# Kernel optimization log

Hardware: AMD Instinct MI355X
Metric: run time of the kernel (lower is better)

The kernel has to match this reference:

```python
import jax, jax.numpy as jnp
import numpy as np

B, S, HID = 2, 2048, 4096
H, KVH, D = 32, 8, 128
MAXPOS = 4096


def _rotate_half(x):
    x1, x2 = jnp.split(x, 2, axis=-1)
    return jnp.concatenate([-x2, x1], axis=-1)


def setup_inputs() -> dict:
    key = jax.random.key(0)
    k0, k1, k2, k3, k4 = jax.random.split(key, 5)
    s = 0.02
    hidden_states = jax.random.normal(k0, (B, S, HID), jnp.float32)
    Wq = jax.random.normal(k1, (HID, H * D), jnp.float32) * s
    Wk = jax.random.normal(k2, (HID, KVH * D), jnp.float32) * s
    Wv = jax.random.normal(k3, (HID, KVH * D), jnp.float32) * s
    Wo = jax.random.normal(k4, (H * D, HID), jnp.float32) * s
    past_key_value = jnp.zeros((B, 2, KVH, MAXPOS, D), jnp.float32)
    # RoPE tables (fp32, as asserted in the torch module)
    inv_freq = 1.0 / (10000.0 ** (np.arange(0, D, 2, dtype=np.float64) / D))
    freqs = np.outer(np.arange(S, dtype=np.float64), inv_freq)  # [S, D/2]
    emb = np.concatenate([freqs, freqs], axis=-1)                # [S, D]
    cos = jnp.asarray(np.cos(emb), jnp.float32)
    sin = jnp.asarray(np.sin(emb), jnp.float32)
    return {"hidden_states": hidden_states, "past_key_value": past_key_value,
            "cos": cos, "sin": sin, "Wq": Wq, "Wk": Wk, "Wv": Wv, "Wo": Wo}


def reference(hidden_states, past_key_value, cos, sin, Wq, Wk, Wv, Wo):
    b, s, _ = hidden_states.shape
    # QKV projections (no bias, as in Llama-style attention)
    q = (hidden_states @ Wq).reshape(b, s, H, D)
    k = (hidden_states @ Wk).reshape(b, s, KVH, D)
    v = (hidden_states @ Wv).reshape(b, s, KVH, D)
    # Fused RoPE (qk_norm is identity for standard models)
    c = cos[None, :, None, :]
    sn = sin[None, :, None, :]
    q = q * c + _rotate_half(q) * sn
    k = k * c + _rotate_half(k) * sn
    # KV-cache update (prefill: context_lengths=0, kvcache_start_index=0)
    k_bhsd = k.transpose(0, 2, 1, 3)  # [b, kvh, s, d]
    v_bhsd = v.transpose(0, 2, 1, 3)
    present = past_key_value.at[:, 0, :, :s, :].set(k_bhsd)
    present = present.at[:, 1, :, :s, :].set(v_bhsd)
    # GQA: repeat kv heads to match query heads
    rep = H // KVH
    kr = jnp.repeat(k, rep, axis=2)  # [b, s, H, d]
    vr = jnp.repeat(v, rep, axis=2)
    scores = jnp.einsum("bqhd,bkhd->bhqk", q, kr) / np.float32(np.sqrt(D))
    causal = jnp.tril(jnp.ones((s, s), bool))  # [q, k]
    scores = jnp.where(causal[None, None], scores, jnp.finfo(scores.dtype).min)
    w = jax.nn.softmax(scores.astype(jnp.float32), axis=-1).astype(q.dtype)
    attn = jnp.einsum("bhqk,bkhd->bqhd", w, vr).reshape(b, s, H * D)
    out = attn @ Wo
    return out, present
```

## Files before the change

kernel.cpp:

```cpp
#include <hip/hip_runtime.h>
#include <hip/hip_bf16.h>

typedef unsigned short u16;
typedef __bf16 bf16x8 __attribute__((ext_vector_type(8)));
typedef float  f32x4  __attribute__((ext_vector_type(4)));

__device__ __forceinline__ u16 f2bf(float f) {
    return __builtin_bit_cast(u16, (__bf16)f);
}
__device__ __forceinline__ float b2f(u16 u) {
    return __builtin_bit_cast(float, (unsigned)u << 16);
}
__device__ __forceinline__ f32x4 mfma16(bf16x8 a, bf16x8 b, f32x4 c) {
    return __builtin_amdgcn_mfma_f32_16x16x32_bf16(a, b, c, 0, 0, 0);
}
__device__ __forceinline__ void gl_lds16(const void* g, void* l) {
    __builtin_amdgcn_global_load_lds((const __attribute__((address_space(1))) void*)g,
                                     (__attribute__((address_space(3))) void*)l, 16, 0, 0);
}

__global__ void k_pre(const float* __restrict__ hidden, u16* __restrict__ hiddenB,
                      const float4* __restrict__ past, float4* __restrict__ present4) {
    int bx = blockIdx.x;
    if (bx < 16384) {
        long i = ((long)bx * 256 + threadIdx.x) * 4;
        float4 v = *(const float4*)(hidden + i);
        ushort4 o;
        o.x = f2bf(v.x); o.y = f2bf(v.y); o.z = f2bf(v.z); o.w = f2bf(v.w);
        *(ushort4*)(hiddenB + i) = o;
    } else {
        long i = (long)(bx - 16384) * 256 + threadIdx.x;
        long g = i >> 16;
        long inner = i & 65535;
        long off = g * 131072 + 65536 + inner;
        present4[off] = past[off];
    }
}

__global__ void k_transpose_all(const float* __restrict__ Wq, const float* __restrict__ Wk,
                                const float* __restrict__ Wv, const float* __restrict__ Wo,
                                u16* __restrict__ WqkvT, u16* __restrict__ WoT) {
    __shared__ float t[32][33];
    const int bx = blockIdx.x, k0 = blockIdx.y * 32;
    const float* src; u16* dst; int N; int col;
    if (bx < 128)      { src = Wq; N = 4096; col = bx * 32;         dst = WqkvT; }
    else if (bx < 160) { src = Wk; N = 1024; col = (bx - 128) * 32; dst = WqkvT + 4096L * 4096; }
    else if (bx < 192) { src = Wv; N = 1024; col = (bx - 160) * 32; dst = WqkvT + 5120L * 4096; }
    else               { src = Wo; N = 4096; col = (bx - 192) * 32; dst = WoT; }
    const int tx = threadIdx.x, ty = threadIdx.y;
    #pragma unroll
    for (int i = 0; i < 32; i += 8)
        t[ty + i][tx] = src[(long)(k0 + ty + i) * N + col + tx];
    __syncthreads();
    #pragma unroll
    for (int i = 0; i < 32; i += 8)
        dst[(long)(col + ty + i) * 4096 + k0 + tx] = f2bf(t[tx][ty + i]);
}

#define ABAR() do { __builtin_amdgcn_sched_barrier(0); __builtin_amdgcn_s_barrier(); \
                    __builtin_amdgcn_sched_barrier(0); } while (0)
#define LGKM0() do { asm volatile("s_waitcnt lgkmcnt(0)" ::: "memory"); \
                     __builtin_amdgcn_sched_barrier(0); } while (0)

__global__ void __launch_bounds__(512, 2)
k_gemm8ph(const u16* __restrict__ A, const u16* __restrict__ Bt,
          float* __restrict__ C, int M, int N, int K, int gx)
{
    extern __shared__ u16 lds[];
    const int nwg = gridDim.x;
    const int bid = blockIdx.x;
    const int swzb = (bid & 7) * (nwg >> 3) + (bid >> 3);
    const long m0 = (long)(swzb / gx) * 256;
    const long n0 = (long)(swzb % gx) * 256;

    const int t = threadIdx.x;
    const int l = t & 63;
    const int w = t >> 6;
    const int wm = w >> 2, wn = w & 3;

    const int srow = t >> 3;
    const int scol = ((t & 7) ^ (srow & 7)) << 3;
    const u16* aph[2] = { A  + (m0 + 0   + srow) * (long)K + scol,
                          A  + (m0 + 128 + srow) * (long)K + scol };
    const u16* bph[2] = { Bt + (n0 + 0   + srow) * (long)K + scol,
                          Bt + (n0 + 128 + srow) * (long)K + scol };

    const int swz0 = (((l >> 4) ^ (l & 7)) << 3);
    const int swz1 = ((((l >> 4) | 4) ^ (l & 7)) << 3);
    const int arowb = (wm * 64 + (l & 15)) * 64;
    const int browb = (wn * 32 + (l & 15)) * 64;

    f32x4 acc[8][4];
    #pragma unroll
    for (int i = 0; i < 8; ++i)
        #pragma unroll
        for (int j = 0; j < 4; ++j) acc[i][j] = (f32x4){0.f, 0.f, 0.f, 0.f};

    bf16x8 a[4][2], b0[2][2], b1[2][2];

    auto stA = [&](int d, int h, int kt) {
        const u16* s = aph[h] + (long)kt * 64;
        gl_lds16(s,              &lds[(d * 2 + h) * 8192 + t * 8]);
        gl_lds16(s + 64L * K,    &lds[(d * 2 + h) * 8192 + 4096 + t * 8]);
    };
    auto stB = [&](int d, int h, int kt) {
        const u16* s = bph[h] + (long)kt * 64;
        gl_lds16(s,              &lds[32768 + (d * 2 + h) * 8192 + t * 8]);
        gl_lds16(s + 64L * K,    &lds[32768 + (d * 2 + h) * 8192 + 4096 + t * 8]);
    };
    auto rdA = [&](int d, int h) {
        const int base = (d * 2 + h) * 8192;
        #pragma unroll
        for (int mf = 0; mf < 4; ++mf) {
            a[mf][0] = *(const bf16x8*)&lds[base + arowb + mf * 1024 + swz0];
            a[mf][1] = *(const bf16x8*)&lds[base + arowb + mf * 1024 + swz1];
        }
    };
    auto rdB = [&](int d, int h, bf16x8 (&bb)[2][2]) {
        const int base = 32768 + (d * 2 + h) * 8192;
        #pragma unroll
        for (int nf = 0; nf < 2; ++nf) {
            bb[nf][0] = *(const bf16x8*)&lds[base + browb + nf * 1024 + swz0];
            bb[nf][1] = *(const bf16x8*)&lds[base + browb + nf * 1024 + swz1];
        }
    };
    auto mfmaQ = [&](int qm, int qn, bf16x8 (&bb)[2][2]) {
        __builtin_amdgcn_s_setprio(1);
        #pragma unroll
        for (int mf = 0; mf < 4; ++mf)
            #pragma unroll
            for (int nf = 0; nf < 2; ++nf) {
                acc[qm * 4 + mf][qn * 2 + nf] =
                    mfma16(a[mf][0], bb[nf][0], acc[qm * 4 + mf][qn * 2 + nf]);
                acc[qm * 4 + mf][qn * 2 + nf] =
                    mfma16(a[mf][1], bb[nf][1], acc[qm * 4 + mf][qn * 2 + nf]);
            }
        __builtin_amdgcn_s_setprio(0);
        __builtin_amdgcn_sched_barrier(0);
    };

    const int nt = K >> 6;
    stA(0, 0, 0); stB(0, 0, 0); stB(0, 1, 0); stA(0, 1, 0);
    stA(1, 0, 1); stB(1, 0, 1); stB(1, 1, 1); stA(1, 1, 1);
    asm volatile("s_waitcnt vmcnt(8)" ::: "memory");
    __builtin_amdgcn_sched_barrier(0);
    __builtin_amdgcn_s_barrier();
    __builtin_amdgcn_sched_barrier(0);

    for (int kt = 0; kt < nt; kt += 2) {
        const bool g = (kt + 2) < nt;
        #pragma unroll
        for (int hh = 0; hh < 2; ++hh) {
            const int d = hh;
            const int ktp = kt + 2 + hh;
            rdA(d, 0); rdB(d, 0, b0);
            ABAR(); LGKM0();
            mfmaQ(0, 0, b0);
            ABAR();
            rdB(d, 1, b1);
            if (g) { stA(d, 0, ktp); stB(d, 0, ktp); }
            ABAR(); LGKM0();
            mfmaQ(0, 1, b1);
            ABAR();
            rdA(d, 1);
            if (g) stB(d, 1, ktp);
            ABAR(); LGKM0();
            mfmaQ(1, 0, b0);
            ABAR();
            if (g) {
                stA(d, 1, ktp);
                asm volatile("s_waitcnt vmcnt(8)" ::: "memory");
            } else {
                asm volatile("s_waitcnt vmcnt(0)" ::: "memory");
            }
            ABAR();
            mfmaQ(1, 1, b1);
            ABAR();
        }
    }

    #pragma unroll
    for (int i8 = 0; i8 < 8; ++i8) {
        const int qm = i8 >> 2, mf = i8 & 3;
        #pragma unroll
        for (int j4 = 0; j4 < 4; ++j4) {
            const int qn = j4 >> 1, nf = j4 & 1;
            long row = m0 + qm * 128 + wm * 64 + mf * 16 + ((l >> 4) << 2);
            float* cp = C + row * N + n0 + qn * 128 + wn * 32 + nf * 16 + (l & 15);
            #pragma unroll
            for (int r = 0; r < 4; ++r) cp[(long)r * N] = acc[i8][j4][r];
        }
    }
}

template<int BNF, int OBF16>
__global__ void __launch_bounds__(512, 2)
k_gemm8(const u16* __restrict__ A, const u16* __restrict__ Bt,
        void* __restrict__ Cv, int M, int N, int K, int gx)
{
    extern __shared__ u16 lds[];
    const int nwg = gridDim.x;
    const int bid = blockIdx.x;
    const int swzb = (bid & 7) * (nwg >> 3) + (bid >> 3);
    const long m0 = (long)(swzb / gx) * 256;
    const long n0 = (long)(swzb % gx) * (64 * BNF);

    const int t = threadIdx.x;
    const int l = t & 63;
    const int w = t >> 6;
    const int wm = w >> 2, wn = w & 3;

    const int srow = t >> 3;
    const int scol = ((t & 7) ^ (srow & 7)) << 3;
    const u16* ap = A  + (m0 + srow) * (long)K + scol;
    const u16* bp = Bt + (n0 + srow) * (long)K + scol;
    const int sL = t * 8;

    const int swz0 = (((l >> 4) ^ (l & 7)) << 3);
    const int swz1 = ((((l >> 4) | 4) ^ (l & 7)) << 3);
    const int arow = wm * 128 + (l & 15);
    const int aoff0 = arow * 64 + swz0, aoff1 = arow * 64 + swz1;
    const int brow = wn * (16 * BNF) + (l & 15);
    const int boff0 = brow * 64 + swz0, boff1 = brow * 64 + swz1;

    f32x4 acc[8][BNF];
    #pragma unroll
    for (int i = 0; i < 8; ++i)
        #pragma unroll
        for (int j = 0; j < BNF; ++j) acc[i][j] = (f32x4){0.f, 0.f, 0.f, 0.f};

    const int nt = K >> 6;
    #pragma unroll
    for (int k = 0; k < 4; ++k)
        gl_lds16(ap + (long)k * 64 * K, &lds[sL + 4096 * k]);
    #pragma unroll
    for (int k = 0; k < BNF; ++k)
        gl_lds16(bp + (long)k * 64 * K, &lds[32768 + sL + 4096 * k]);

    for (int kt = 0; kt < nt; ++kt) {
        const int d = kt & 1;
        const int dA = d * 16384, dB = 32768 + d * 4096 * BNF;
        if (kt + 1 < nt) {
            const int e = d ^ 1;
            const u16* a1 = ap + (kt + 1) * 64;
            const u16* b1 = bp + (kt + 1) * 64;
            #pragma unroll
            for (int k = 0; k < 4; ++k)
                gl_lds16(a1 + (long)k * 64 * K, &lds[e * 16384 + sL + 4096 * k]);
            #pragma unroll
            for (int k = 0; k < BNF; ++k)
                gl_lds16(b1 + (long)k * 64 * K, &lds[32768 + e * 4096 * BNF + sL + 4096 * k]);
            if constexpr (BNF == 3) asm volatile("s_waitcnt vmcnt(7)" ::: "memory");
            else                    asm volatile("s_waitcnt vmcnt(8)" ::: "memory");
        } else {
            asm volatile("s_waitcnt vmcnt(0)" ::: "memory");
        }
        ABAR();

        bf16x8 bfr[BNF][2];
        #pragma unroll
        for (int nf = 0; nf < BNF; ++nf) {
            bfr[nf][0] = *(const bf16x8*)&lds[dB + boff0 + nf * 1024];
            bfr[nf][1] = *(const bf16x8*)&lds[dB + boff1 + nf * 1024];
        }
        {
            bf16x8 af[2][2];
            #pragma unroll
            for (int mm = 0; mm < 2; ++mm) {
                af[mm][0] = *(const bf16x8*)&lds[dA + aoff0 + mm * 1024];
                af[mm][1] = *(const bf16x8*)&lds[dA + aoff1 + mm * 1024];
            }
            LGKM0();
            __builtin_amdgcn_s_setprio(1);
            #pragma unroll
            for (int mm = 0; mm < 2; ++mm)
                #pragma unroll
                for (int nf = 0; nf < BNF; ++nf) {
                    acc[mm][nf] = mfma16(af[mm][0], bfr[nf][0], acc[mm][nf]);
                    acc[mm][nf] = mfma16(af[mm][1], bfr[nf][1], acc[mm][nf]);
                }
            __builtin_amdgcn_s_setprio(0);
            __builtin_amdgcn_sched_barrier(0);
        }
        #pragma unroll
        for (int q = 1; q < 4; ++q) {
            bf16x8 af[2][2];
            #pragma unroll
            for (int mm = 0; mm < 2; ++mm) {
                af[mm][0] = *(const bf16x8*)&lds[dA + aoff0 + (q * 2 + mm) * 1024];
                af[mm][1] = *(const bf16x8*)&lds[dA + aoff1 + (q * 2 + mm) * 1024];
            }
            ABAR();
            LGKM0();
            __builtin_amdgcn_s_setprio(1);
            #pragma unroll
            for (int mm = 0; mm < 2; ++mm)
                #pragma unroll
                for (int nf = 0; nf < BNF; ++nf) {
                    acc[q * 2 + mm][nf] = mfma16(af[mm][0], bfr[nf][0], acc[q * 2 + mm][nf]);
                    acc[q * 2 + mm][nf] = mfma16(af[mm][1], bfr[nf][1], acc[q * 2 + mm][nf]);
                }
            __builtin_amdgcn_s_setprio(0);
            __builtin_amdgcn_sched_barrier(0);
        }
        ABAR();
    }

    #pragma unroll
    for (int mf = 0; mf < 8; ++mf)
        #pragma unroll
        for (int nf = 0; nf < BNF; ++nf) {
            long row = m0 + wm * 128 + mf * 16 + ((l >> 4) << 2);
            long cb = row * N + n0 + wn * (16 * BNF) + nf * 16 + (l & 15);
            if constexpr (OBF16) {
                u16* cp = (u16*)Cv + cb;
                #pragma unroll
                for (int r = 0; r < 4; ++r) cp[(long)r * N] = f2bf(acc[mf][nf][r]);
            } else {
                float* cp = (float*)Cv + cb;
                #pragma unroll
                for (int r = 0; r < 4; ++r) cp[(long)r * N] = acc[mf][nf][r];
            }
        }
}

__global__ void k_rope_scatter(const u16* __restrict__ qkv, const float* __restrict__ cosb,
                               const float* __restrict__ sinb, u16* __restrict__ Qb,
                               u16* __restrict__ Kb, u16* __restrict__ Vt,
                               float* __restrict__ present)
{
    long idx = (long)blockIdx.x * 256 + threadIdx.x;
    int pg   = (int)(idx & 15);
    int rem  = (int)(idx >> 4);
    int slot = rem % 48;
    int tok  = rem / 48;
    int b = tok >> 11, s = tok & 2047;
    int pair = pg * 4;

    const u16* base = qkv + (long)tok * 6144 + slot * 128 + pair;
    ushort4 xu1 = *(const ushort4*)(base);
    ushort4 xu2 = *(const ushort4*)(base + 64);
    float4 x1 = {b2f(xu1.x), b2f(xu1.y), b2f(xu1.z), b2f(xu1.w)};
    float4 x2 = {b2f(xu2.x), b2f(xu2.y), b2f(xu2.z), b2f(xu2.w)};

    if (slot < 40) {
        float4 c  = *(const float4*)(cosb + s * 128 + pair);
        float4 sn = *(const float4*)(sinb + s * 128 + pair);
        float4 y1, y2;
        y1.x = x1.x * c.x - x2.x * sn.x;  y2.x = x2.x * c.x + x1.x * sn.x;
        y1.y = x1.y * c.y - x2.y * sn.y;  y2.y = x2.y * c.y + x1.y * sn.y;
        y1.z = x1.z * c.z - x2.z * sn.z;  y2.z = x2.z * c.z + x1.z * sn.z;
        y1.w = x1.w * c.w - x2.w * sn.w;  y2.w = x2.w * c.w + x1.w * sn.w;
        if (slot < 32) {
            const float sc = 0.0883883476483184f;
            long qoff = (((long)b * 32 + slot) * 2048 + s) * 128 + pair;
            ushort4 o1, o2;
            o1.x = f2bf(y1.x * sc); o1.y = f2bf(y1.y * sc);
            o1.z = f2bf(y1.z * sc); o1.w = f2bf(y1.w * sc);
            o2.x = f2bf(y2.x * sc); o2.y = f2bf(y2.y * sc);
            o2.z = f2bf(y2.z * sc); o2.w = f2bf(y2.w * sc);
            *(ushort4*)(Qb + qoff)      = o1;
            *(ushort4*)(Qb + qoff + 64) = o2;
        } else {
            int kvh = slot - 32;
            long koff = (((long)b * 8 + kvh) * 2048 + s) * 128 + pair;
            ushort4 o1, o2;
            o1.x = f2bf(y1.x); o1.y = f2bf(y1.y); o1.z = f2bf(y1.z); o1.w = f2bf(y1.w);
            o2.x = f2bf(y2.x); o2.y = f2bf(y2.y); o2.z = f2bf(y2.z); o2.w = f2bf(y2.w);
            *(ushort4*)(Kb + koff)      = o1;
            *(ushort4*)(Kb + koff + 64) = o2;
            long poff = ((((long)b * 2 + 0) * 8 + kvh) * 4096 + s) * 128 + pair;
            *(float4*)(present + poff)      = y1;
            *(float4*)(present + poff + 64) = y2;
        }
    } else {
        int kvh = slot - 40;
        long poff = ((((long)b * 2 + 1) * 8 + kvh) * 4096 + s) * 128 + pair;
        *(float4*)(present + poff)      = x1;
        *(float4*)(present + poff + 64) = x2;
        long voff = (((long)b * 8 + kvh) * 128 + pair) * 2048 + s;
        Vt[voff]             = xu1.x;
        Vt[voff + 1 * 2048]  = xu1.y;
        Vt[voff + 2 * 2048]  = xu1.z;
        Vt[voff + 3 * 2048]  = xu1.w;
        Vt[voff + 64 * 2048] = xu2.x;
        Vt[voff + 65 * 2048] = xu2.y;
        Vt[voff + 66 * 2048] = xu2.z;
        Vt[voff + 67 * 2048] = xu2.w;
    }
}

__global__ void __launch_bounds__(256, 2)
k_attn(const u16* __restrict__ Qb, const u16* __restrict__ Kb,
       const u16* __restrict__ Vt, u16* __restrict__ attnB)
{
    __shared__ __align__(16) u16 Ks[64 * 128];
    __shared__ __align__(16) u16 Vs[128 * 64];
    const int l = threadIdx.x & 63;
    const int w = threadIdx.x >> 6;
    const int h = blockIdx.y, b = blockIdx.z;
    const int p = blockIdx.x;
    const int kvh = h >> 2;
    u16* Psw = &Ks[w * 2048];

    const long kbase = ((long)b * 8 + kvh) * (2048L * 128);
    const long vbase = ((long)b * 8 + kvh) * (128L * 2048);
    f32x4 zero = {0.f, 0.f, 0.f, 0.f};

    for (int half = 0; half < 2; ++half) {
        const int qt = half ? (15 - p) : p;
        const int q0 = qt * 128;

        const long qbase = (((long)b * 32 + h) * 2048 + q0 + w * 32) * 128;
        bf16x8 qf[2][4];
        #pragma unroll
        for (int mi = 0; mi < 2; ++mi)
            #pragma unroll
            for (int kk = 0; kk < 4; ++kk)
                qf[mi][kk] = *(const bf16x8*)(Qb + qbase + (long)(mi * 16 + (l & 15)) * 128
                                              + kk * 32 + ((l >> 4) << 3));

        f32x4 o[2][8];
        float mst[2][4], lst[2][4];
        #pragma unroll
        for (int mi = 0; mi < 2; ++mi) {
            #pragma unroll
            for (int j = 0; j < 8; ++j) o[mi][j] = zero;
            #pragma unroll
            for (int r = 0; r < 4; ++r) { mst[mi][r] = -3.0e38f; lst[mi][r] = 0.f; }
        }

        const int nkt = (q0 >> 6) + 2;
        for (int kt = 0; kt < nkt; ++kt) {
            const int k0 = kt * 64;
            __syncthreads();
            #pragma unroll
            for (int i = 0; i < 4; ++i) {
                int c = w * 4 + i;
                int row = c * 4 + (l >> 4);
                int lg = ((l & 15) ^ (row & 15)) << 3;
                gl_lds16(Kb + kbase + (long)(k0 + row) * 128 + lg, &Ks[c * 512]);
            }
            #pragma unroll
            for (int i = 0; i < 4; ++i) {
                int c = w * 4 + i;
                int row = c * 8 + (l >> 3);
                int lg = ((l & 7) ^ (row & 7)) << 3;
                gl_lds16(Vt + vbase + (long)row * 2048 + k0 + lg, &Vs[c * 512]);
            }
            __syncthreads();

            f32x4 s[2][4];
            #pragma unroll
            for (int mi = 0; mi < 2; ++mi)
                #pragma unroll
                for (int nf = 0; nf < 4; ++nf) s[mi][nf] = zero;
            #pragma unroll
            for (int kk = 0; kk < 4; ++kk) {
                bf16x8 kf[4];
                #pragma unroll
                for (int nf = 0; nf < 4; ++nf) {
                    int row = nf * 16 + (l & 15);
                    int ph = (kk * 4 + (l >> 4)) ^ (row & 15);
                    kf[nf] = *(const bf16x8*)&Ks[row * 128 + ph * 8];
                }
                __builtin_amdgcn_s_setprio(1);
                #pragma unroll
                for (int mi = 0; mi < 2; ++mi)
                    #pragma unroll
                    for (int nf = 0; nf < 4; ++nf)
                        s[mi][nf] = mfma16(qf[mi][kk], kf[nf], s[mi][nf]);
                __builtin_amdgcn_s_setprio(0);
            }
            #pragma unroll
            for (int mi = 0; mi < 2; ++mi)
                #pragma unroll
                for (int nf = 0; nf < 4; ++nf)
                    #pragma unroll
                    for (int r = 0; r < 4; ++r) {
                        int rowg = q0 + w * 32 + mi * 16 + ((l >> 4) << 2) + r;
                        int colg = k0 + nf * 16 + (l & 15);
                        if (colg > rowg) s[mi][nf][r] = -1.0e30f;
                    }
            #pragma unroll
            for (int mi = 0; mi < 2; ++mi)
                #pragma unroll
                for (int r = 0; r < 4; ++r) {
                    float t = fmaxf(fmaxf(s[mi][0][r], s[mi][1][r]),
                                    fmaxf(s[mi][2][r], s[mi][3][r]));
                    t = fmaxf(t, __shfl_xor(t, 1));
                    t = fmaxf(t, __shfl_xor(t, 2));
                    t = fmaxf(t, __shfl_xor(t, 4));
                    t = fmaxf(t, __shfl_xor(t, 8));
                    float nm = fmaxf(mst[mi][r], t);
                    float sc = __expf(mst[mi][r] - nm);
                    mst[mi][r] = nm;
                    lst[mi][r] *= sc;
                    #pragma unroll
                    for (int nf2 = 0; nf2 < 8; ++nf2) o[mi][nf2][r] *= sc;
                }
            __syncthreads();
            #pragma unroll
            for (int mi = 0; mi < 2; ++mi)
                #pragma unroll
                for (int nf = 0; nf < 4; ++nf)
                    #pragma unroll
                    for (int r = 0; r < 4; ++r) {
                        float pv = __expf(s[mi][nf][r] - mst[mi][r]);
                        lst[mi][r] += pv;
                        int row = mi * 16 + ((l >> 4) << 2) + r;
                        int col = nf * 16 + (l & 15);
                        Psw[row * 64 + (((col >> 3) ^ (row & 7)) << 3) + (col & 7)] = f2bf(pv);
                    }
            #pragma unroll
            for (int kk2 = 0; kk2 < 2; ++kk2) {
                bf16x8 pa[2];
                #pragma unroll
                for (int mi = 0; mi < 2; ++mi) {
                    int row = mi * 16 + (l & 15);
                    int ph = (kk2 * 4 + (l >> 4)) ^ (row & 7);
                    pa[mi] = *(const bf16x8*)&Psw[row * 64 + ph * 8];
                }
                #pragma unroll
                for (int nf2 = 0; nf2 < 8; ++nf2) {
                    int vrow = nf2 * 16 + (l & 15);
                    int ph = (kk2 * 4 + (l >> 4)) ^ (vrow & 7);
                    bf16x8 vf = *(const bf16x8*)&Vs[vrow * 64 + ph * 8];
                    __builtin_amdgcn_s_setprio(1);
                    #pragma unroll
                    for (int mi = 0; mi < 2; ++mi)
                        o[mi][nf2] = mfma16(pa[mi], vf, o[mi][nf2]);
                    __builtin_amdgcn_s_setprio(0);
                }
            }
        }

        #pragma unroll
        for (int mi = 0; mi < 2; ++mi)
            #pragma unroll
            for (int r = 0; r < 4; ++r) {
                float t = lst[mi][r];
                t += __shfl_xor(t, 1);
                t += __shfl_xor(t, 2);
                t += __shfl_xor(t, 4);
                t += __shfl_xor(t, 8);
                lst[mi][r] = 1.0f / t;
            }
        #pragma unroll
        for (int mi = 0; mi < 2; ++mi)
            #pragma unroll
            for (int nf2 = 0; nf2 < 8; ++nf2)
                #pragma unroll
                for (int r = 0; r < 4; ++r) {
                    long row = (long)b * 2048 + q0 + w * 32 + mi * 16 + ((l >> 4) << 2) + r;
                    attnB[row * 4096 + h * 128 + nf2 * 16 + (l & 15)] =
                        f2bf(o[mi][nf2][r] * lst[mi][r]);
                }
    }
}

extern "C" void kernel_launch(void* const* d_in, const int* in_sizes, int n_in,
                              void* d_out, int out_size, void* d_ws, size_t ws_size,
                              hipStream_t stream)
{
    (void)in_sizes; (void)n_in; (void)out_size; (void)ws_size;
    const float* hidden = (const float*)d_in[0];
    const float* past   = (const float*)d_in[1];
    const float* cosb   = (const float*)d_in[2];
    const float* sinb   = (const float*)d_in[3];
    const float* Wq     = (const float*)d_in[4];
    const float* Wk     = (const float*)d_in[5];
    const float* Wv     = (const float*)d_in[6];
    const float* Wo     = (const float*)d_in[7];
    float* out     = (float*)d_out;
    float* present = out + 16777216L;

    char* ws = (char*)d_ws;
    u16*  hiddenB = (u16*)(ws);
    u16*  WqkvT   = (u16*)(ws + 33554432L);
    u16*  WoT     = (u16*)(ws + 83886080L);
    u16*  QKVb    = (u16*)(ws + 117440512L);
    u16*  Kb      = (u16*)(ws + 218103808L);
    u16*  Vt      = (u16*)(ws + 226492416L);
    u16*  Qbuf    = hiddenB;
    u16*  attnB   = QKVb;

    static bool attr_done = false;
    if (!attr_done) {
        hipFuncSetAttribute((const void*)k_gemm8<3, 1>,
                            hipFuncAttributeMaxDynamicSharedMemorySize, 114688);
        hipFuncSetAttribute((const void*)k_gemm8ph,
                            hipFuncAttributeMaxDynamicSharedMemorySize, 131072);
        attr_done = true;
    }

    k_pre<<<24576, 256, 0, stream>>>(hidden, hiddenB, (const float4*)past, (float4*)present);
    k_transpose_all<<<dim3(320, 128), dim3(32, 8), 0, stream>>>(Wq, Wk, Wv, Wo, WqkvT, WoT);
    k_gemm8<3, 1><<<512, 512, 114688, stream>>>(hiddenB, WqkvT, (void*)QKVb,
                                                4096, 6144, 4096, 32);
    k_rope_scatter<<<12288, 256, 0, stream>>>(QKVb, cosb, sinb, Qbuf, Kb, Vt, present);
    k_attn<<<dim3(8, 32, 2), 256, 0, stream>>>(Qbuf, Kb, Vt, attnB);
    k_gemm8ph<<<256, 512, 131072, stream>>>(attnB, WoT, out, 4096, 4096, 4096, 16);
}
```

Before: 581.1 us.

## Split-K QKV projection with 256x256 tile kernel and sum partials in RoPE

The QKV projection now runs on the 256x256-tile GEMM kernel, templated to emit bf16 and split K in two. This launches 768 workgroups (384 tiles × 2 K halves), each writing a separate bf16 partial buffer. The RoPE/scatter kernel reads both partials and sums them before applying rotation and writing K, V and present. The old 256x192 GEMM kernel is removed. The intent is better CU load balance and the faster tile schedule, at the cost of twice the intermediate write/read traffic and extra bf16 rounding of each partial.

```diff
diff --git a/kernel.cpp b/kernel.cpp
--- a/kernel.cpp
+++ b/kernel.cpp
@@ -62,16 +62,22 @@
 #define LGKM0() do { asm volatile("s_waitcnt lgkmcnt(0)" ::: "memory"); \
                      __builtin_amdgcn_sched_barrier(0); } while (0)
 
+template<int OBF16, int NSPLIT>
 __global__ void __launch_bounds__(512, 2)
 k_gemm8ph(const u16* __restrict__ A, const u16* __restrict__ Bt,
-          float* __restrict__ C, int M, int N, int K, int gx)
+          void* __restrict__ Cv, int M, int N, int K, int gx)
 {
     extern __shared__ u16 lds[];
     const int nwg = gridDim.x;
     const int bid = blockIdx.x;
     const int swzb = (bid & 7) * (nwg >> 3) + (bid >> 3);
-    const long m0 = (long)(swzb / gx) * 256;
-    const long n0 = (long)(swzb % gx) * 256;
+    const int tiles = nwg / NSPLIT;
+    const int half = swzb / tiles;
+    const int tile = swzb % tiles;
+    const long m0 = (long)(tile / gx) * 256;
+    const long n0 = (long)(tile % gx) * 256;
+    const int Klen = K / NSPLIT;
+    const long kbase = (long)half * Klen;
 
     const int t = threadIdx.x;
     const int l = t & 63;
@@ -80,10 +86,10 @@
 
     const int srow = t >> 3;
     const int scol = ((t & 7) ^ (srow & 7)) << 3;
-    const u16* aph[2] = { A  + (m0 + 0   + srow) * (long)K + scol,
-                          A  + (m0 + 128 + srow) * (long)K + scol };
-    const u16* bph[2] = { Bt + (n0 + 0   + srow) * (long)K + scol,
-                          Bt + (n0 + 128 + srow) * (long)K + scol };
+    const u16* aph[2] = { A  + (m0 + 0   + srow) * (long)K + kbase + scol,
+                          A  + (m0 + 128 + srow) * (long)K + kbase + scol };
+    const u16* bph[2] = { Bt + (n0 + 0   + srow) * (long)K + kbase + scol,
+                          Bt + (n0 + 128 + srow) * (long)K + kbase + scol };
 
     const int swz0 = (((l >> 4) ^ (l & 7)) << 3);
     const int swz1 = ((((l >> 4) | 4) ^ (l & 7)) << 3);
@@ -139,7 +145,7 @@
         __builtin_amdgcn_sched_barrier(0);
     };
 
-    const int nt = K >> 6;
+    const int nt = Klen >> 6;
     stA(0, 0, 0); stB(0, 0, 0); stB(0, 1, 0); stA(0, 1, 0);
     stA(1, 0, 1); stB(1, 0, 1); stB(1, 1, 1); stA(1, 1, 1);
     asm volatile("s_waitcnt vmcnt(8)" ::: "memory");
@@ -186,149 +192,26 @@
         for (int j4 = 0; j4 < 4; ++j4) {
             const int qn = j4 >> 1, nf = j4 & 1;
             long row = m0 + qm * 128 + wm * 64 + mf * 16 + ((l >> 4) << 2);
-            float* cp = C + row * N + n0 + qn * 128 + wn * 32 + nf * 16 + (l & 15);
-            #pragma unroll
-            for (int r = 0; r < 4; ++r) cp[(long)r * N] = acc[i8][j4][r];
-        }
-    }
-}
-
-template<int BNF, int OBF16>
-__global__ void __launch_bounds__(512, 2)
-k_gemm8(const u16* __restrict__ A, const u16* __restrict__ Bt,
-        void* __restrict__ Cv, int M, int N, int K, int gx)
-{
-    extern __shared__ u16 lds[];
-    const int nwg = gridDim.x;
-    const int bid = blockIdx.x;
-    const int swzb = (bid & 7) * (nwg >> 3) + (bid >> 3);
-    const long m0 = (long)(swzb / gx) * 256;
-    const long n0 = (long)(swzb % gx) * (64 * BNF);
-
-    const int t = threadIdx.x;
-    const int l = t & 63;
-    const int w = t >> 6;
-    const int wm = w >> 2, wn = w & 3;
-
-    const int srow = t >> 3;
-    const int scol = ((t & 7) ^ (srow & 7)) << 3;
-    const u16* ap = A  + (m0 + srow) * (long)K + scol;
-    const u16* bp = Bt + (n0 + srow) * (long)K + scol;
-    const int sL = t * 8;
-
-    const int swz0 = (((l >> 4) ^ (l & 7)) << 3);
-    const int swz1 = ((((l >> 4) | 4) ^ (l & 7)) << 3);
-    const int arow = wm * 128 + (l & 15);
-    const int aoff0 = arow * 64 + swz0, aoff1 = arow * 64 + swz1;
-    const int brow = wn * (16 * BNF) + (l & 15);
-    const int boff0 = brow * 64 + swz0, boff1 = brow * 64 + swz1;
-
-    f32x4 acc[8][BNF];
-    #pragma unroll
-    for (int i = 0; i < 8; ++i)
-        #pragma unroll
-        for (int j = 0; j < BNF; ++j) acc[i][j] = (f32x4){0.f, 0.f, 0.f, 0.f};
-
-    const int nt = K >> 6;
-    #pragma unroll
-    for (int k = 0; k < 4; ++k)
-        gl_lds16(ap + (long)k * 64 * K, &lds[sL + 4096 * k]);
-    #pragma unroll
-    for (int k = 0; k < BNF; ++k)
-        gl_lds16(bp + (long)k * 64 * K, &lds[32768 + sL + 4096 * k]);
-
-    for (int kt = 0; kt < nt; ++kt) {
-        const int d = kt & 1;
-        const int dA = d * 16384, dB = 32768 + d * 4096 * BNF;
-        if (kt + 1 < nt) {
-            const int e = d ^ 1;
-            const u16* a1 = ap + (kt + 1) * 64;
-            const u16* b1 = bp + (kt + 1) * 64;
-            #pragma unroll
-            for (int k = 0; k < 4; ++k)
-                gl_lds16(a1 + (long)k * 64 * K, &lds[e * 16384 + sL + 4096 * k]);
-            #pragma unroll
-            for (int k = 0; k < BNF; ++k)
-                gl_lds16(b1 + (long)k * 64 * K, &lds[32768 + e * 4096 * BNF + sL + 4096 * k]);
-            if constexpr (BNF == 3) asm volatile("s_waitcnt vmcnt(7)" ::: "memory");
-            else                    asm volatile("s_waitcnt vmcnt(8)" ::: "memory");
-        } else {
-            asm volatile("s_waitcnt vmcnt(0)" ::: "memory");
-        }
-        ABAR();
-
-        bf16x8 bfr[BNF][2];
-        #pragma unroll
-        for (int nf = 0; nf < BNF; ++nf) {
-            bfr[nf][0] = *(const bf16x8*)&lds[dB + boff0 + nf * 1024];
-            bfr[nf][1] = *(const bf16x8*)&lds[dB + boff1 + nf * 1024];
-        }
-        {
-            bf16x8 af[2][2];
-            #pragma unroll
-            for (int mm = 0; mm < 2; ++mm) {
-                af[mm][0] = *(const bf16x8*)&lds[dA + aoff0 + mm * 1024];
-                af[mm][1] = *(const bf16x8*)&lds[dA + aoff1 + mm * 1024];
-            }
-            LGKM0();
-            __builtin_amdgcn_s_setprio(1);
-            #pragma unroll
-            for (int mm = 0; mm < 2; ++mm)
-                #pragma unroll
-                for (int nf = 0; nf < BNF; ++nf) {
-                    acc[mm][nf] = mfma16(af[mm][0], bfr[nf][0], acc[mm][nf]);
-                    acc[mm][nf] = mfma16(af[mm][1], bfr[nf][1], acc[mm][nf]);
-                }
-            __builtin_amdgcn_s_setprio(0);
-            __builtin_amdgcn_sched_barrier(0);
-        }
-        #pragma unroll
-        for (int q = 1; q < 4; ++q) {
-            bf16x8 af[2][2];
-            #pragma unroll
-            for (int mm = 0; mm < 2; ++mm) {
-                af[mm][0] = *(const bf16x8*)&lds[dA + aoff0 + (q * 2 + mm) * 1024];
-                af[mm][1] = *(const bf16x8*)&lds[dA + aoff1 + (q * 2 + mm) * 1024];
-            }
-            ABAR();
-            LGKM0();
-            __builtin_amdgcn_s_setprio(1);
-            #pragma unroll
-            for (int mm = 0; mm < 2; ++mm)
-                #pragma unroll
-                for (int nf = 0; nf < BNF; ++nf) {
-                    acc[q * 2 + mm][nf] = mfma16(af[mm][0], bfr[nf][0], acc[q * 2 + mm][nf]);
-                    acc[q * 2 + mm][nf] = mfma16(af[mm][1], bfr[nf][1], acc[q * 2 + mm][nf]);
-                }
-            __builtin_amdgcn_s_setprio(0);
-            __builtin_amdgcn_sched_barrier(0);
-        }
-        ABAR();
-    }
-
-    #pragma unroll
-    for (int mf = 0; mf < 8; ++mf)
-        #pragma unroll
-        for (int nf = 0; nf < BNF; ++nf) {
-            long row = m0 + wm * 128 + mf * 16 + ((l >> 4) << 2);
-            long cb = row * N + n0 + wn * (16 * BNF) + nf * 16 + (l & 15);
+            long cb = row * N + n0 + qn * 128 + wn * 32 + nf * 16 + (l & 15);
             if constexpr (OBF16) {
-                u16* cp = (u16*)Cv + cb;
-                #pragma unroll
-                for (int r = 0; r < 4; ++r) cp[(long)r * N] = f2bf(acc[mf][nf][r]);
+                u16* cp = (u16*)Cv + (long)half * M * N + cb;
+                #pragma unroll
+                for (int r = 0; r < 4; ++r) cp[(long)r * N] = f2bf(acc[i8][j4][r]);
             } else {
                 float* cp = (float*)Cv + cb;
                 #pragma unroll
-                for (int r = 0; r < 4; ++r) cp[(long)r * N] = acc[mf][nf][r];
-            }
-        }
-}
-
-__global__ void k_rope_scatter(const u16* __restrict__ qkv, const float* __restrict__ cosb,
+                for (int r = 0; r < 4; ++r) cp[(long)r * N] = acc[i8][j4][r];
+            }
+        }
+    }
+}
+
+__global__ void k_rope_scatter(const u16* __restrict__ qkvH, const float* __restrict__ cosb,
                                const float* __restrict__ sinb, u16* __restrict__ Qb,
                                u16* __restrict__ Kb, u16* __restrict__ Vt,
                                float* __restrict__ present)
 {
+    const long HSTR = 25165824L;
     long idx = (long)blockIdx.x * 256 + threadIdx.x;
     int pg   = (int)(idx & 15);
     int rem  = (int)(idx >> 4);
@@ -337,11 +220,15 @@
     int b = tok >> 11, s = tok & 2047;
     int pair = pg * 4;
 
-    const u16* base = qkv + (long)tok * 6144 + slot * 128 + pair;
-    ushort4 xu1 = *(const ushort4*)(base);
-    ushort4 xu2 = *(const ushort4*)(base + 64);
-    float4 x1 = {b2f(xu1.x), b2f(xu1.y), b2f(xu1.z), b2f(xu1.w)};
-    float4 x2 = {b2f(xu2.x), b2f(xu2.y), b2f(xu2.z), b2f(xu2.w)};
+    const u16* base = qkvH + (long)tok * 6144 + slot * 128 + pair;
+    ushort4 p0a = *(const ushort4*)(base);
+    ushort4 p0b = *(const ushort4*)(base + 64);
+    ushort4 p1a = *(const ushort4*)(base + HSTR);
+    ushort4 p1b = *(const ushort4*)(base + HSTR + 64);
+    float4 x1 = {b2f(p0a.x) + b2f(p1a.x), b2f(p0a.y) + b2f(p1a.y),
+                 b2f(p0a.z) + b2f(p1a.z), b2f(p0a.w) + b2f(p1a.w)};
+    float4 x2 = {b2f(p0b.x) + b2f(p1b.x), b2f(p0b.y) + b2f(p1b.y),
+                 b2f(p0b.z) + b2f(p1b.z), b2f(p0b.w) + b2f(p1b.w)};
 
     if (slot < 40) {
         float4 c  = *(const float4*)(cosb + s * 128 + pair);
@@ -379,14 +266,14 @@
         *(float4*)(present + poff)      = x1;
         *(float4*)(present + poff + 64) = x2;
         long voff = (((long)b * 8 + kvh) * 128 + pair) * 2048 + s;
-        Vt[voff]             = xu1.x;
-        Vt[voff + 1 * 2048]  = xu1.y;
-        Vt[voff + 2 * 2048]  = xu1.z;
-        Vt[voff + 3 * 2048]  = xu1.w;
-        Vt[voff + 64 * 2048] = xu2.x;
-        Vt[voff + 65 * 2048] = xu2.y;
-        Vt[voff + 66 * 2048] = xu2.z;
-        Vt[voff + 67 * 2048] = xu2.w;
+        Vt[voff]             = f2bf(x1.x);
+        Vt[voff + 1 * 2048]  = f2bf(x1.y);
+        Vt[voff + 2 * 2048]  = f2bf(x1.z);
+        Vt[voff + 3 * 2048]  = f2bf(x1.w);
+        Vt[voff + 64 * 2048] = f2bf(x2.x);
+        Vt[voff + 65 * 2048] = f2bf(x2.y);
+        Vt[voff + 66 * 2048] = f2bf(x2.z);
+        Vt[voff + 67 * 2048] = f2bf(x2.w);
     }
 }
 
@@ -579,26 +466,27 @@
     u16*  hiddenB = (u16*)(ws);
     u16*  WqkvT   = (u16*)(ws + 33554432L);
     u16*  WoT     = (u16*)(ws + 83886080L);
-    u16*  QKVb    = (u16*)(ws + 117440512L);
+    u16*  QKVh    = (u16*)(ws + 117440512L);
     u16*  Kb      = (u16*)(ws + 218103808L);
     u16*  Vt      = (u16*)(ws + 226492416L);
     u16*  Qbuf    = hiddenB;
-    u16*  attnB   = QKVb;
+    u16*  attnB   = QKVh;
 
     static bool attr_done = false;
     if (!attr_done) {
-        hipFuncSetAttribute((const void*)k_gemm8<3, 1>,
-                            hipFuncAttributeMaxDynamicSharedMemorySize, 114688);
-        hipFuncSetAttribute((const void*)k_gemm8ph,
+        hipFuncSetAttribute((const void*)k_gemm8ph<1, 2>,
+                            hipFuncAttributeMaxDynamicSharedMemorySize, 131072);
+        hipFuncSetAttribute((const void*)k_gemm8ph<0, 1>,
                             hipFuncAttributeMaxDynamicSharedMemorySize, 131072);
         attr_done = true;
     }
 
     k_pre<<<24576, 256, 0, stream>>>(hidden, hiddenB, (const float4*)past, (float4*)present);
     k_transpose_all<<<dim3(320, 128), dim3(32, 8), 0, stream>>>(Wq, Wk, Wv, Wo, WqkvT, WoT);
-    k_gemm8<3, 1><<<512, 512, 114688, stream>>>(hiddenB, WqkvT, (void*)QKVb,
-                                                4096, 6144, 4096, 32);
-    k_rope_scatter<<<12288, 256, 0, stream>>>(QKVb, cosb, sinb, Qbuf, Kb, Vt, present);
+    k_gemm8ph<1, 2><<<768, 512, 131072, stream>>>(hiddenB, WqkvT, (void*)QKVh,
+                                                  4096, 6144, 4096, 24);
+    k_rope_scatter<<<12288, 256, 0, stream>>>(QKVh, cosb, sinb, Qbuf, Kb, Vt, present);
     k_attn<<<dim3(8, 32, 2), 256, 0, stream>>>(Qbuf, Kb, Vt, attnB);
-    k_gemm8ph<<<256, 512, 131072, stream>>>(attnB, WoT, out, 4096, 4096, 4096, 16);
-}
+    k_gemm8ph<0, 1><<<256, 512, 131072, stream>>>(attnB, WoT, (void*)out,
+                                                  4096, 4096, 4096, 16);
+}
```

Result: no change. 575.9 us (-0.9%).
